# Optimization experiments

Measured on AMD Instinct MI355X. Metric: run time of the kernel, lower is better.

Reference implementation:

```python
import jax, jax.numpy as jnp
import numpy as np

N_HEADS = 16

def setup_inputs() -> dict:
    key = jax.random.key(0)
    qkv = jax.random.normal(key, (4, 3072, 1024), dtype=jnp.float32)
    return {"qkv": qkv}

def reference(qkv):
    bs, width, length = qkv.shape
    ch = width // (3 * N_HEADS)
    qkv_h = qkv.reshape(bs * N_HEADS, 3 * ch, length)
    q, k, v = jnp.split(qkv_h, 3, axis=1)  # each [bs*H, ch, T]
    scale = 1.0 / jnp.sqrt(jnp.sqrt(jnp.asarray(ch, qkv.dtype)))
    # [bs*H, T, T] scores
    weight = jnp.einsum('bct,bcs->bts', q * scale, k * scale)
    weight = jax.nn.softmax(weight.astype(jnp.float32), axis=-1).astype(weight.dtype)
    a = jnp.einsum('bts,bcs->bct', weight, v)  # [bs*H, ch, T]
    return a.reshape(bs, -1, length)
```

## Files before the change

### kernel.cpp

```cpp
#include <hip/hip_runtime.h>
#include <hip/hip_bf16.h>


typedef __bf16 bf16_8 __attribute__((ext_vector_type(8)));
typedef __bf16 bf16_4 __attribute__((ext_vector_type(4)));
typedef float floatx4 __attribute__((ext_vector_type(4)));

#define NTHREADS 512
#define STR 64
#define NSTEPS 16

#if __has_builtin(__builtin_amdgcn_exp2f)
#define EXP2(x) __builtin_amdgcn_exp2f(x)
#else
#define EXP2(x) exp2f(x)
#endif
#define QSCALE 0.18033688011112042f

#define LDS_BYTES 57344

__device__ __forceinline__ int kap(int row) { return ((row >> 1) + (row >> 4)) & 7; }

__device__ __forceinline__ unsigned pk_bf16(float a, float b) {
    unsigned r;
    asm("v_cvt_pk_bf16_f32 %0, %1, %2" : "=v"(r) : "v"(a), "v"(b));
    return r;
}
__device__ __forceinline__ void swap32(unsigned& x, unsigned& y) {
    asm("v_permlane32_swap_b32 %0, %1" : "+v"(x), "+v"(y));
}
__device__ __forceinline__ void swap16(unsigned& x, unsigned& y) {
    asm("v_permlane16_swap_b32 %0, %1" : "+v"(x), "+v"(y));
}

__device__ __forceinline__ void write_k(__bf16* kn, const float4* r, int si, int sG) {
    #pragma unroll
    for (int rr = 0; rr < 4; ++rr) {
        int srow = si * 4 + rr;
        bf16_4 w;
        w[0] = (__bf16)((const float*)&r[0])[rr];
        w[1] = (__bf16)((const float*)&r[1])[rr];
        w[2] = (__bf16)((const float*)&r[2])[rr];
        w[3] = (__bf16)((const float*)&r[3])[rr];
        *(bf16_4*)&kn[srow * STR + ((sG ^ (kap(srow) << 1)) << 2)] = w;
    }
}
__device__ __forceinline__ void write_v(__bf16* vn, const float4* r, int si, int c0) {
    #pragma unroll
    for (int jj = 0; jj < 4; ++jj) {
        int c = c0 + jj;
        bf16_4 w;
        w[0] = (__bf16)r[jj].x; w[1] = (__bf16)r[jj].y;
        w[2] = (__bf16)r[jj].z; w[3] = (__bf16)r[jj].w;
        *(bf16_4*)&vn[c * STR + ((si ^ (kap(c) << 1)) << 2)] = w;
    }
}

__global__ __launch_bounds__(NTHREADS, 4)
void attn_kernel(const float* __restrict__ qkv, float* __restrict__ out) {
    __shared__ char smem[LDS_BYTES];
    __bf16* q_s = (__bf16*)smem;
    __bf16* k0  = (__bf16*)(smem + 16384);
    __bf16* k1  = (__bf16*)(smem + 24576);
    __bf16* v0  = (__bf16*)(smem + 32768);
    __bf16* v1  = (__bf16*)(smem + 40960);
    __bf16* v2  = (__bf16*)(smem + 49152);

    const int tid  = threadIdx.x;
    const int wave = tid >> 6;
    const int lane = tid & 63;
    const int quad = lane >> 4;
    const int i16  = lane & 15;

    const int bx = blockIdx.x;
    const int bh = bx & 63;
    const int t0 = (bx >> 6) << 7;

    const float* qg = qkv + (size_t)bh * 196608;
    const float* kg = qg + 65536;
    const float* vg = qg + 131072;

    const int sv = tid >> 8;
    const int st = tid & 255;
    const int si = st & 15;
    const int sG = st >> 4;
    const int c0 = sG << 2;
    const float* gsrc = sv ? vg : kg;

    {
        const int cG = tid >> 5;
        const int ti = tid & 31;
        float4 q4[4];
        #pragma unroll
        for (int jj = 0; jj < 4; ++jj)
            q4[jj] = *(const float4*)(qg + (cG * 4 + jj) * 1024 + t0 + ti * 4);
        #pragma unroll
        for (int rr = 0; rr < 4; ++rr) {
            int trow = ti * 4 + rr;
            bf16_4 w;
            w[0] = (__bf16)(((const float*)&q4[0])[rr] * QSCALE);
            w[1] = (__bf16)(((const float*)&q4[1])[rr] * QSCALE);
            w[2] = (__bf16)(((const float*)&q4[2])[rr] * QSCALE);
            w[3] = (__bf16)(((const float*)&q4[3])[rr] * QSCALE);
            *(bf16_4*)&q_s[trow * STR + ((cG ^ (kap(trow) << 1)) << 2)] = w;
        }
    }
    {
        float4 r4[4];
        #pragma unroll
        for (int jj = 0; jj < 4; ++jj)
            r4[jj] = *(const float4*)(gsrc + (c0 + jj) * 1024 + si * 4);
        if (!sv) write_k(k0, r4, si, sG);
        else     write_v(v0, r4, si, c0);
    }
    __syncthreads();

    bf16_8 qf[2];
    {
        int row = wave * 16 + i16;
        int x = kap(row);
        #pragma unroll
        for (int kk = 0; kk < 2; ++kk)
            qf[kk] = *(const bf16_8*)&q_s[row * STR + ((((kk << 2) | quad) ^ x) << 3)];
    }

    floatx4 O[4];
    #pragma unroll
    for (int cn = 0; cn < 4; ++cn) O[cn] = (floatx4){0.f, 0.f, 0.f, 0.f};
    float l = 0.f;

    bf16_8 afp[2];
    int vprev = 2, vcur = 0, vnext = 1;

    for (int is = 0; is < NSTEPS; ++is) {
        const __bf16* kc = (is & 1) ? k1 : k0;

        float4 pr[4];
        if (is < NSTEPS - 1) {
            const int s0n = (is + 1) * 64;
            #pragma unroll
            for (int jj = 0; jj < 4; ++jj)
                pr[jj] = *(const float4*)(gsrc + (c0 + jj) * 1024 + s0n + si * 4);
        }

        floatx4 St[4];
        #pragma unroll
        for (int sb = 0; sb < 4; ++sb) {
            int srow = sb * 16 + i16;
            int x = (sb + (i16 >> 1)) & 7;
            bf16_8 kf0 = *(const bf16_8*)&kc[srow * STR + ((quad ^ x) << 3)];
            bf16_8 kf1 = *(const bf16_8*)&kc[srow * STR + (((4 | quad) ^ x) << 3)];
            floatx4 a = (floatx4){0.f, 0.f, 0.f, 0.f};
            a = __builtin_amdgcn_mfma_f32_16x16x32_bf16(kf0, qf[0], a, 0, 0, 0);
            a = __builtin_amdgcn_mfma_f32_16x16x32_bf16(kf1, qf[1], a, 0, 0, 0);
            St[sb] = a;
        }

        unsigned c01[4], c23[4];
        #pragma unroll
        for (int sb = 0; sb < 4; ++sb) {
            float p0 = EXP2(St[sb][0]);
            float p1 = EXP2(St[sb][1]);
            float p2 = EXP2(St[sb][2]);
            float p3 = EXP2(St[sb][3]);
            l += (p0 + p1) + (p2 + p3);
            c01[sb] = pk_bf16(p0, p1);
            c23[sb] = pk_bf16(p2, p3);
        }
        bf16_8 af[2];
        #pragma unroll
        for (int kk = 0; kk < 2; ++kk) {
            unsigned x0 = c01[2 * kk], y0 = c01[2 * kk + 1];
            unsigned x1 = c23[2 * kk], y1 = c23[2 * kk + 1];
            swap32(x0, y0); swap16(x0, y0);
            swap32(x1, y1); swap16(x1, y1);
            union { unsigned u[4]; bf16_8 v; } t;
            t.u[0] = x0; t.u[1] = x1; t.u[2] = y0; t.u[3] = y1;
            af[kk] = t.v;
        }

        if (is > 0) {
            const __bf16* vp = (vprev == 0) ? v0 : ((vprev == 1) ? v1 : v2);
            #pragma unroll
            for (int cn = 0; cn < 4; ++cn) {
                int crow = cn * 16 + i16;
                int xc = (cn + (i16 >> 1)) & 7;
                #pragma unroll
                for (int kk = 0; kk < 2; ++kk) {
                    bf16_8 vf = *(const bf16_8*)&vp[crow * STR + ((((kk << 2) | quad) ^ xc) << 3)];
                    O[cn] = __builtin_amdgcn_mfma_f32_16x16x32_bf16(vf, afp[kk], O[cn], 0, 0, 0);
                }
            }
        }
        afp[0] = af[0]; afp[1] = af[1];

        if (is < NSTEPS - 1) {
            if (!sv) {
                __bf16* kn = (is & 1) ? k0 : k1;
                write_k(kn, pr, si, sG);
            } else {
                __bf16* vn = (vnext == 0) ? v0 : ((vnext == 1) ? v1 : v2);
                write_v(vn, pr, si, c0);
            }
            __syncthreads();
        }
        vprev = vcur; vcur = vnext; vnext = (vnext == 2) ? 0 : vnext + 1;
    }

    {
        const __bf16* vp = (vprev == 0) ? v0 : ((vprev == 1) ? v1 : v2);
        #pragma unroll
        for (int cn = 0; cn < 4; ++cn) {
            int crow = cn * 16 + i16;
            int xc = (cn + (i16 >> 1)) & 7;
            #pragma unroll
            for (int kk = 0; kk < 2; ++kk) {
                bf16_8 vf = *(const bf16_8*)&vp[crow * STR + ((((kk << 2) | quad) ^ xc) << 3)];
                O[cn] = __builtin_amdgcn_mfma_f32_16x16x32_bf16(vf, afp[kk], O[cn], 0, 0, 0);
            }
        }
    }

    float s = l;
    s += __shfl_xor(s, 16);
    s += __shfl_xor(s, 32);
    const float linv = 1.0f / s;
    float* og = out + (size_t)bh * 65536 + t0 + wave * 16;
    #pragma unroll
    for (int cn = 0; cn < 4; ++cn)
        #pragma unroll
        for (int r = 0; r < 4; ++r)
            og[(cn * 16 + 4 * quad + r) * 1024 + i16] = O[cn][r] * linv;
}

extern "C" void kernel_launch(void* const* d_in, const int* in_sizes, int n_in,
                              void* d_out, int out_size, void* d_ws, size_t ws_size,
                              hipStream_t stream) {
    const float* qkv = (const float*)d_in[0];
    float* out = (float*)d_out;
    attn_kernel<<<dim3(512), dim3(NTHREADS), 0, stream>>>(qkv, out);
}
```

Measured before the change: 103.1 us.

## Switch attention to 32x32x16 MFMA with split-key waves and LDS reduction

Replaces the 16x16x32 MFMA tiles with 32x32x16 MFMAs. Each pair of waves now shares a 32-query block and splits the 64-key step into two halves. K rows are permuted in LDS so the score accumulator layout maps straight onto the PV operand, which removes the permlane swaps. The two waves' partial outputs and row sums are combined through LDS at the end, at the cost of an extra barrier, a shared-memory round trip, and only half the waves writing output.

```diff
diff --git a/kernel.cpp b/kernel.cpp
--- a/kernel.cpp
+++ b/kernel.cpp
@@ -5,6 +5,7 @@
 typedef __bf16 bf16_8 __attribute__((ext_vector_type(8)));
 typedef __bf16 bf16_4 __attribute__((ext_vector_type(4)));
 typedef float floatx4 __attribute__((ext_vector_type(4)));
+typedef float floatx16 __attribute__((ext_vector_type(16)));
 
 #define NTHREADS 512
 #define STR 64
@@ -19,30 +20,32 @@
 
 #define LDS_BYTES 57344
 
+#define ZERO16 (floatx16){0.f,0.f,0.f,0.f,0.f,0.f,0.f,0.f,0.f,0.f,0.f,0.f,0.f,0.f,0.f,0.f}
+
 __device__ __forceinline__ int kap(int row) { return ((row >> 1) + (row >> 4)) & 7; }
+__device__ __forceinline__ int sigma_row(int s) {
+    return (s & 0x33) | ((s & 4) << 1) | ((s & 8) >> 1);
+}
 
 __device__ __forceinline__ unsigned pk_bf16(float a, float b) {
     unsigned r;
     asm("v_cvt_pk_bf16_f32 %0, %1, %2" : "=v"(r) : "v"(a), "v"(b));
     return r;
 }
-__device__ __forceinline__ void swap32(unsigned& x, unsigned& y) {
-    asm("v_permlane32_swap_b32 %0, %1" : "+v"(x), "+v"(y));
-}
-__device__ __forceinline__ void swap16(unsigned& x, unsigned& y) {
-    asm("v_permlane16_swap_b32 %0, %1" : "+v"(x), "+v"(y));
-}
+
+union U8 { unsigned u[4]; bf16_8 v; };
 
 __device__ __forceinline__ void write_k(__bf16* kn, const float4* r, int si, int sG) {
     #pragma unroll
     for (int rr = 0; rr < 4; ++rr) {
         int srow = si * 4 + rr;
+        int m = sigma_row(srow);
         bf16_4 w;
         w[0] = (__bf16)((const float*)&r[0])[rr];
         w[1] = (__bf16)((const float*)&r[1])[rr];
         w[2] = (__bf16)((const float*)&r[2])[rr];
         w[3] = (__bf16)((const float*)&r[3])[rr];
-        *(bf16_4*)&kn[srow * STR + ((sG ^ (kap(srow) << 1)) << 2)] = w;
+        *(bf16_4*)&kn[m * STR + ((sG ^ (kap(m) << 1)) << 2)] = w;
     }
 }
 __device__ __forceinline__ void write_v(__bf16* vn, const float4* r, int si, int c0) {
@@ -69,8 +72,10 @@
     const int tid  = threadIdx.x;
     const int wave = tid >> 6;
     const int lane = tid & 63;
-    const int quad = lane >> 4;
-    const int i16  = lane & 15;
+    const int hv   = lane >> 5;
+    const int l31  = lane & 31;
+    const int g    = wave >> 1;
+    const int sh   = wave & 1;
 
     const int bx = blockIdx.x;
     const int bh = bx & 63;
@@ -115,25 +120,27 @@
     }
     __syncthreads();
 
-    bf16_8 qf[2];
-    {
-        int row = wave * 16 + i16;
+    bf16_8 qf[4];
+    {
+        int row = g * 32 + l31;
         int x = kap(row);
         #pragma unroll
-        for (int kk = 0; kk < 2; ++kk)
-            qf[kk] = *(const bf16_8*)&q_s[row * STR + ((((kk << 2) | quad) ^ x) << 3)];
-    }
-
-    floatx4 O[4];
-    #pragma unroll
-    for (int cn = 0; cn < 4; ++cn) O[cn] = (floatx4){0.f, 0.f, 0.f, 0.f};
+        for (int kc = 0; kc < 4; ++kc)
+            qf[kc] = *(const bf16_8*)&q_s[row * STR + ((((kc << 1) | hv) ^ x) << 3)];
+    }
+
+    floatx16 O0 = ZERO16, O1 = ZERO16;
     float l = 0.f;
-
-    bf16_8 afp[2];
+    bf16_8 pfp0, pfp1;
     int vprev = 2, vcur = 0, vnext = 1;
 
+    const int krow = sh * 32 + l31;
+    const int kx   = kap(krow);
+    const int vx0  = kap(l31);
+    const int vx1  = kap(32 + l31);
+
     for (int is = 0; is < NSTEPS; ++is) {
-        const __bf16* kc = (is & 1) ? k1 : k0;
+        const __bf16* kb = (is & 1) ? k1 : k0;
 
         float4 pr[4];
         if (is < NSTEPS - 1) {
@@ -143,56 +150,44 @@
                 pr[jj] = *(const float4*)(gsrc + (c0 + jj) * 1024 + s0n + si * 4);
         }
 
-        floatx4 St[4];
-        #pragma unroll
-        for (int sb = 0; sb < 4; ++sb) {
-            int srow = sb * 16 + i16;
-            int x = (sb + (i16 >> 1)) & 7;
-            bf16_8 kf0 = *(const bf16_8*)&kc[srow * STR + ((quad ^ x) << 3)];
-            bf16_8 kf1 = *(const bf16_8*)&kc[srow * STR + (((4 | quad) ^ x) << 3)];
-            floatx4 a = (floatx4){0.f, 0.f, 0.f, 0.f};
-            a = __builtin_amdgcn_mfma_f32_16x16x32_bf16(kf0, qf[0], a, 0, 0, 0);
-            a = __builtin_amdgcn_mfma_f32_16x16x32_bf16(kf1, qf[1], a, 0, 0, 0);
-            St[sb] = a;
-        }
-
-        unsigned c01[4], c23[4];
-        #pragma unroll
-        for (int sb = 0; sb < 4; ++sb) {
-            float p0 = EXP2(St[sb][0]);
-            float p1 = EXP2(St[sb][1]);
-            float p2 = EXP2(St[sb][2]);
-            float p3 = EXP2(St[sb][3]);
-            l += (p0 + p1) + (p2 + p3);
-            c01[sb] = pk_bf16(p0, p1);
-            c23[sb] = pk_bf16(p2, p3);
-        }
-        bf16_8 af[2];
-        #pragma unroll
-        for (int kk = 0; kk < 2; ++kk) {
-            unsigned x0 = c01[2 * kk], y0 = c01[2 * kk + 1];
-            unsigned x1 = c23[2 * kk], y1 = c23[2 * kk + 1];
-            swap32(x0, y0); swap16(x0, y0);
-            swap32(x1, y1); swap16(x1, y1);
-            union { unsigned u[4]; bf16_8 v; } t;
-            t.u[0] = x0; t.u[1] = x1; t.u[2] = y0; t.u[3] = y1;
-            af[kk] = t.v;
-        }
+        floatx16 St = ZERO16;
+        #pragma unroll
+        for (int kc = 0; kc < 4; ++kc) {
+            bf16_8 kf = *(const bf16_8*)&kb[krow * STR + ((((kc << 1) | hv) ^ kx) << 3)];
+            St = __builtin_amdgcn_mfma_f32_32x32x16_bf16(kf, qf[kc], St, 0, 0, 0);
+        }
+
+        U8 w0, w1;
+        #pragma unroll
+        for (int d = 0; d < 4; ++d) {
+            float pa = EXP2(St[2 * d]);
+            float pb = EXP2(St[2 * d + 1]);
+            float pc = EXP2(St[8 + 2 * d]);
+            float pd = EXP2(St[8 + 2 * d + 1]);
+            l += (pa + pb) + (pc + pd);
+            w0.u[d] = pk_bf16(pa, pb);
+            w1.u[d] = pk_bf16(pc, pd);
+        }
+        bf16_8 pfn0 = w0.v, pfn1 = w1.v;
 
         if (is > 0) {
             const __bf16* vp = (vprev == 0) ? v0 : ((vprev == 1) ? v1 : v2);
-            #pragma unroll
-            for (int cn = 0; cn < 4; ++cn) {
-                int crow = cn * 16 + i16;
-                int xc = (cn + (i16 >> 1)) & 7;
-                #pragma unroll
-                for (int kk = 0; kk < 2; ++kk) {
-                    bf16_8 vf = *(const bf16_8*)&vp[crow * STR + ((((kk << 2) | quad) ^ xc) << 3)];
-                    O[cn] = __builtin_amdgcn_mfma_f32_16x16x32_bf16(vf, afp[kk], O[cn], 0, 0, 0);
-                }
-            }
-        }
-        afp[0] = af[0]; afp[1] = af[1];
+            {
+                int vrow = l31;
+                bf16_8 vfa = *(const bf16_8*)&vp[vrow * STR + ((((sh << 2) | hv) ^ vx0) << 3)];
+                O0 = __builtin_amdgcn_mfma_f32_32x32x16_bf16(vfa, pfp0, O0, 0, 0, 0);
+                bf16_8 vfb = *(const bf16_8*)&vp[vrow * STR + ((((sh << 2) | 2 | hv) ^ vx0) << 3)];
+                O0 = __builtin_amdgcn_mfma_f32_32x32x16_bf16(vfb, pfp1, O0, 0, 0, 0);
+            }
+            {
+                int vrow = 32 + l31;
+                bf16_8 vfa = *(const bf16_8*)&vp[vrow * STR + ((((sh << 2) | hv) ^ vx1) << 3)];
+                O1 = __builtin_amdgcn_mfma_f32_32x32x16_bf16(vfa, pfp0, O1, 0, 0, 0);
+                bf16_8 vfb = *(const bf16_8*)&vp[vrow * STR + ((((sh << 2) | 2 | hv) ^ vx1) << 3)];
+                O1 = __builtin_amdgcn_mfma_f32_32x32x16_bf16(vfb, pfp1, O1, 0, 0, 0);
+            }
+        }
+        pfp0 = pfn0; pfp1 = pfn1;
 
         if (is < NSTEPS - 1) {
             if (!sv) {
@@ -209,28 +204,56 @@
 
     {
         const __bf16* vp = (vprev == 0) ? v0 : ((vprev == 1) ? v1 : v2);
-        #pragma unroll
-        for (int cn = 0; cn < 4; ++cn) {
-            int crow = cn * 16 + i16;
-            int xc = (cn + (i16 >> 1)) & 7;
+        {
+            int vrow = l31;
+            bf16_8 vfa = *(const bf16_8*)&vp[vrow * STR + ((((sh << 2) | hv) ^ vx0) << 3)];
+            O0 = __builtin_amdgcn_mfma_f32_32x32x16_bf16(vfa, pfp0, O0, 0, 0, 0);
+            bf16_8 vfb = *(const bf16_8*)&vp[vrow * STR + ((((sh << 2) | 2 | hv) ^ vx0) << 3)];
+            O0 = __builtin_amdgcn_mfma_f32_32x32x16_bf16(vfb, pfp1, O0, 0, 0, 0);
+        }
+        {
+            int vrow = 32 + l31;
+            bf16_8 vfa = *(const bf16_8*)&vp[vrow * STR + ((((sh << 2) | hv) ^ vx1) << 3)];
+            O1 = __builtin_amdgcn_mfma_f32_32x32x16_bf16(vfa, pfp0, O1, 0, 0, 0);
+            bf16_8 vfb = *(const bf16_8*)&vp[vrow * STR + ((((sh << 2) | 2 | hv) ^ vx1) << 3)];
+            O1 = __builtin_amdgcn_mfma_f32_32x32x16_bf16(vfb, pfp1, O1, 0, 0, 0);
+        }
+    }
+
+    l += __shfl_xor(l, 32);
+
+    __syncthreads();
+    float* xo = (float*)smem;
+    float* xl = (float*)(smem + 40960);
+    if (sh == 1) {
+        float* b = xo + g * 2048;
+        #pragma unroll
+        for (int rq = 0; rq < 4; ++rq) {
+            floatx4 a0 = {O0[4 * rq], O0[4 * rq + 1], O0[4 * rq + 2], O0[4 * rq + 3]};
+            *(floatx4*)&b[(rq * 64 + lane) * 4] = a0;
+            floatx4 a1 = {O1[4 * rq], O1[4 * rq + 1], O1[4 * rq + 2], O1[4 * rq + 3]};
+            *(floatx4*)&b[((4 + rq) * 64 + lane) * 4] = a1;
+        }
+        xl[g * 64 + lane] = l;
+    }
+    __syncthreads();
+    if (sh == 0) {
+        const float* b = xo + g * 2048;
+        const float lt = l + xl[g * 64 + lane];
+        const float linv = 1.0f / lt;
+        float* og = out + (size_t)bh * 65536 + t0 + g * 32;
+        #pragma unroll
+        for (int rq = 0; rq < 4; ++rq) {
+            floatx4 a0 = *(const floatx4*)&b[(rq * 64 + lane) * 4];
+            floatx4 a1 = *(const floatx4*)&b[((4 + rq) * 64 + lane) * 4];
             #pragma unroll
-            for (int kk = 0; kk < 2; ++kk) {
-                bf16_8 vf = *(const bf16_8*)&vp[crow * STR + ((((kk << 2) | quad) ^ xc) << 3)];
-                O[cn] = __builtin_amdgcn_mfma_f32_16x16x32_bf16(vf, afp[kk], O[cn], 0, 0, 0);
-            }
-        }
-    }
-
-    float s = l;
-    s += __shfl_xor(s, 16);
-    s += __shfl_xor(s, 32);
-    const float linv = 1.0f / s;
-    float* og = out + (size_t)bh * 65536 + t0 + wave * 16;
-    #pragma unroll
-    for (int cn = 0; cn < 4; ++cn)
-        #pragma unroll
-        for (int r = 0; r < 4; ++r)
-            og[(cn * 16 + 4 * quad + r) * 1024 + i16] = O[cn][r] * linv;
+            for (int j = 0; j < 4; ++j) {
+                int cl = j + 8 * rq + 4 * hv;
+                og[cl * 1024 + l31] = (O0[4 * rq + j] + a0[j]) * linv;
+                og[(32 + cl) * 1024 + l31] = (O1[4 * rq + j] + a1[j]) * linv;
+            }
+        }
+    }
 }
 
 extern "C" void kernel_launch(void* const* d_in, const int* in_sizes, int n_in,
```

New measurement: 105.5 us. 2.4% more time.
